# Kernel tuning notes

Measured on AMD Instinct MI355X. Metric: run time of the kernel, lower is better.

## Reference

```python
import jax, jax.numpy as jnp
import numpy as np


def _lstm(x, Wx, Wh, b):
    """Fused-gate LSTM over time axis 1. x: [B,T,I]; Wx: [I,4H]; Wh: [H,4H]; b: [4H].
    Gate order (i, f, g, o) as in flax.linen.LSTMCell. Zero initial carry."""
    B, T, _ = x.shape
    H = Wh.shape[0]
    # Precompute all input-to-gate contributions in one big GEMM.
    xg = jnp.einsum('bti,ih->bth', x, Wx) + b  # [B,T,4H]

    def step(carry, xt):
        c, h = carry
        z = xt + h @ Wh  # [B,4H]
        i, f, g, o = jnp.split(z, 4, axis=-1)
        c = jax.nn.sigmoid(f) * c + jax.nn.sigmoid(i) * jnp.tanh(g)
        h = jax.nn.sigmoid(o) * jnp.tanh(c)
        return (c, h), h

    init = (jnp.zeros((B, H), x.dtype), jnp.zeros((B, H), x.dtype))
    _, hs = jax.lax.scan(step, init, jnp.swapaxes(xg, 0, 1))  # hs: [T,B,H]
    return jnp.swapaxes(hs, 0, 1)  # [B,T,H]


def _forward(X, conv_w, conv_b,
             Wx1, Wh1, b1, Wx2, Wh2, b2, Wx3, Wh3, b3, Wx4, Wh4, b4,
             Wa, ba, Va, bva, Wd1, bd1, Wd2, bd2):
    # 1-D conv, SAME padding (flax default), NWC layout.
    x = jax.lax.conv_general_dilated(X, conv_w, (1,), 'SAME',
                                     dimension_numbers=('NWC', 'WIO', 'NWC')) + conv_b
    # NOTE: source uses jnp.flip(..., axis=-1) -> flips FEATURE axis (faithful to source).
    x1 = _lstm(x, Wx1, Wh1, b1)
    x2 = _lstm(jnp.flip(x, axis=-1), Wx2, Wh2, b2)
    x = jnp.concatenate([x1, x2], axis=-1)  # [B,T,2F]
    x1 = _lstm(x, Wx3, Wh3, b3)
    x2 = _lstm(jnp.flip(x, axis=-1), Wx4, Wh4, b4)
    enc = jnp.concatenate([x1, x2], axis=-1)  # [B,T,4F]
    # Additive attention: softmax over time axis.
    score = jnp.tanh(enc @ Wa + ba) @ Va + bva  # [B,T,1]
    w = jax.nn.softmax(score, axis=1)
    ctx = jnp.sum(w * enc, axis=1)  # [B,4F]
    # MLP head (dropout deterministic -> identity).
    h = jnp.tanh(ctx @ Wd1 + bd1)
    return h @ Wd2 + bd2  # [B,1]


def setup_inputs() -> dict:
    key = jax.random.key(0)
    B, T, Cin, F = 32, 4096, 8, 64
    ks = iter(jax.random.split(key, 32))

    def w(shape):
        fan_in = shape[0] if len(shape) <= 2 else shape[0] * shape[1]
        return jax.random.normal(next(ks), shape, jnp.float32) / np.sqrt(fan_in)

    d = {}
    d['X'] = jax.random.normal(next(ks), (B, T, Cin), jnp.float32)
    d['conv_w'] = w((4, Cin, 16))
    d['conv_b'] = jnp.zeros((16,), jnp.float32)
    lstm_dims = {'1': (16, F), '2': (16, F), '3': (2 * F, 2 * F), '4': (2 * F, 2 * F)}
    for n, (i_dim, h_dim) in lstm_dims.items():
        d['Wx' + n] = w((i_dim, 4 * h_dim))
        d['Wh' + n] = w((h_dim, 4 * h_dim))
        d['b' + n] = jnp.zeros((4 * h_dim,), jnp.float32)
    d['Wa'] = w((4 * F, F)); d['ba'] = jnp.zeros((F,), jnp.float32)
    d['Va'] = w((F, 1));     d['bva'] = jnp.zeros((1,), jnp.float32)
    d['Wd1'] = w((4 * F, F)); d['bd1'] = jnp.zeros((F,), jnp.float32)
    d['Wd2'] = w((F, 1));     d['bd2'] = jnp.zeros((1,), jnp.float32)
    d['deterministic'] = 1
    return d


def reference(X, conv_w, conv_b,
              Wx1, Wh1, b1, Wx2, Wh2, b2, Wx3, Wh3, b3, Wx4, Wh4, b4,
              Wa, ba, Va, bva, Wd1, bd1, Wd2, bd2, deterministic):
    # deterministic=1 -> dropout is the identity; already reflected in _forward.
    return _forward(X, conv_w, conv_b,
                    Wx1, Wh1, b1, Wx2, Wh2, b2, Wx3, Wh3, b3, Wx4, Wh4, b4,
                    Wa, ba, Va, bva, Wd1, bd1, Wd2, bd2)
```

## Files before the change

kernel.cpp:

```cpp
#include <hip/hip_runtime.h>


#define TFULL 4096
#define NB 32

__device__ __forceinline__ float fexp2(float x){ return __builtin_amdgcn_exp2f(x); }
__device__ __forceinline__ float frcp(float x){ return __builtin_amdgcn_rcpf(x); }
__device__ __forceinline__ float sigf(float x){ return frcp(1.f + fexp2(-1.44269504f*x)); }
__device__ __forceinline__ float tanh_(float x){
    float e = fexp2(fminf(2.88539008f*x, 126.f));
    return (e - 1.f) * frcp(e + 1.f);
}

__global__ __launch_bounds__(256) void k_init(float* __restrict__ st1,
        float* __restrict__ st2, float* __restrict__ am, float* __restrict__ al,
        float* __restrict__ acc){
    int i = blockIdx.x * 256 + threadIdx.x;
    if (i < 8192)  st1[i] = 0.f;
    if (i < 16384) st2[i] = 0.f;
    if (i < 8192)  acc[i] = 0.f;
    if (i < 32){ am[i] = -3.4e38f; al[i] = 0.f; }
}

__global__ __launch_bounds__(256) void k_pack(
        const float* __restrict__ Wx1, const float* __restrict__ Wh1, const float* __restrict__ b1,
        const float* __restrict__ Wx2, const float* __restrict__ Wh2, const float* __restrict__ b2,
        const float* __restrict__ Wx3, const float* __restrict__ Wh3, const float* __restrict__ b3,
        const float* __restrict__ Wx4, const float* __restrict__ Wh4, const float* __restrict__ b4,
        float* __restrict__ W34, float* __restrict__ b34, float* __restrict__ WhT2,
        float* __restrict__ WhT1, float* __restrict__ WxT1, float* __restrict__ b12){
    int i0 = blockIdx.x * 256 + threadIdx.x;
    int stride = gridDim.x * 256;
    for (int e = i0; e < 131072; e += stride){
        int k = e >> 10, n = e & 1023;
        W34[e] = (n < 512) ? Wx3[k*512 + n] : Wx4[(127 - k)*512 + (n - 512)];
    }
    for (int e = i0; e < 1024; e += stride) b34[e] = (e < 512) ? b3[e] : b4[e - 512];
    for (int e = i0; e < 131072; e += stride){
        int l = e >> 16, r = e & 65535, col = r >> 7, k = r & 127;
        WhT2[e] = (l ? Wh4 : Wh3)[k*512 + col];
    }
    for (int e = i0; e < 32768; e += stride){
        int l = e >> 14, r = e & 16383, col = r >> 6, k = r & 63;
        WhT1[e] = (l ? Wh2 : Wh1)[k*256 + col];
    }
    for (int e = i0; e < 8192; e += stride){
        int l = e >> 12, q = e & 4095, col = q >> 4, r = q & 15;
        WxT1[e] = l ? Wx2[(15 - r)*256 + col] : Wx1[r*256 + col];
    }
    for (int e = i0; e < 512; e += stride) b12[e] = (e < 256) ? b1[e] : b2[e - 256];
}

__global__ __launch_bounds__(256) void k_conv(const float* __restrict__ X,
        const float* __restrict__ W, const float* __restrict__ Bv,
        float* __restrict__ out, int t0, int lc){
    __shared__ float Ws[512];
    __shared__ float bs[16];
    int tid = threadIdx.x;
    Ws[tid] = W[tid]; Ws[tid + 256] = W[tid + 256];
    if (tid < 16) bs[tid] = Bv[tid];
    __syncthreads();
    int m = blockIdx.x * 256 + tid;
    int b = m >> lc, trel = m & ((1 << lc) - 1);
    int t = t0 + trel;
    float o[16];
    #pragma unroll
    for (int co = 0; co < 16; ++co) o[co] = bs[co];
    #pragma unroll
    for (int w = 0; w < 4; ++w){
        int tt = t + w - 1;
        if (tt >= 0 && tt < TFULL){
            const float* xr = X + ((size_t)(b << 12) + tt) * 8;
            #pragma unroll
            for (int ci = 0; ci < 8; ++ci){
                float v = xr[ci];
                #pragma unroll
                for (int co = 0; co < 16; ++co) o[co] += v * Ws[(w*8 + ci)*16 + co];
            }
        }
    }
    float* op = out + (size_t)m * 16;
    #pragma unroll
    for (int q = 0; q < 4; ++q)
        *(float4*)(op + q*4) = make_float4(o[q*4], o[q*4+1], o[q*4+2], o[q*4+3]);
}

__global__ void __launch_bounds__(512)
__attribute__((amdgpu_waves_per_eu(2, 2)))
k_scan1(const float* __restrict__ x,
        const float* __restrict__ WxT1, const float* __restrict__ WhT1,
        const float* __restrict__ b12,
        float* __restrict__ cc, float* __restrict__ st1, int C){
    int l = blockIdx.x >> 5;
    int b = blockIdx.x & 31;
    int j = threadIdx.x;
    int col = j & 255;
    int half = j >> 8;
    float4 wx4[4], wh4[8];
    float bias = 0.f;
    if (half == 0){
        const float4* wp = (const float4*)(WxT1 + ((size_t)l*256 + col)*16);
        #pragma unroll
        for (int i = 0; i < 4; ++i) wx4[i] = wp[i];
        bias = b12[l*256 + col];
    } else {
        #pragma unroll
        for (int i = 0; i < 4; ++i) wx4[i] = make_float4(0.f, 0.f, 0.f, 0.f);
    }
    {
        const float4* wp = (const float4*)(WhT1 + ((size_t)l*256 + col)*64 + half*32);
        #pragma unroll
        for (int i = 0; i < 8; ++i) wh4[i] = wp[i];
    }

    __shared__ float xs[128 * 16];
    __shared__ float zp[512];
    __shared__ float hbufs[64];
    float c = 0.f;
    int sidx = (l*32 + b)*64 + (j & 63);
    if (j < 64){ c = st1[sidx]; hbufs[j] = st1[4096 + sidx]; }
    __syncthreads();

    const float* xb = x + ((size_t)b * C) * 16;
    float* ccb = cc + ((size_t)b * C) * 128 + (l << 6);

    for (int t = 0; t < C; ++t){
        int s = t & 127;
        if (s == 0){
            __syncthreads();
            const float4* src = (const float4*)(xb + (size_t)t * 16);
            float4* dst = (float4*)xs;
            if (t + (j >> 2) < C) dst[j] = src[j];
            __syncthreads();
        }
        float a0 = bias, a1 = 0.f, a2 = 0.f, a3 = 0.f;
        if (half == 0){
            const float4* xr = (const float4*)(xs + s * 16);
            #pragma unroll
            for (int r4 = 0; r4 < 4; ++r4){
                float4 xv = xr[r4];
                a0 = fmaf(xv.x, wx4[r4].x, a0);
                a1 = fmaf(xv.y, wx4[r4].y, a1);
                a2 = fmaf(xv.z, wx4[r4].z, a2);
                a3 = fmaf(xv.w, wx4[r4].w, a3);
            }
        }
        const float4* hb4 = (const float4*)hbufs;
        #pragma unroll
        for (int k4 = 0; k4 < 8; ++k4){
            float4 hv = hb4[(half << 3) + k4];
            a0 = fmaf(hv.x, wh4[k4].x, a0);
            a1 = fmaf(hv.y, wh4[k4].y, a1);
            a2 = fmaf(hv.z, wh4[k4].z, a2);
            a3 = fmaf(hv.w, wh4[k4].w, a3);
        }
        zp[(half << 8) + col] = (a0 + a1) + (a2 + a3);
        __syncthreads();
        if (j < 64){
            float zi = zp[j]       + zp[256 + j];
            float zf = zp[64 + j]  + zp[320 + j];
            float zg = zp[128 + j] + zp[384 + j];
            float zo = zp[192 + j] + zp[448 + j];
            c = sigf(zf) * c + sigf(zi) * tanh_(zg);
            float h = sigf(zo) * tanh_(c);
            hbufs[j] = h;
            ccb[(size_t)t * 128 + j] = h;
        }
        __syncthreads();
    }
    if (j < 64){ st1[sidx] = c; st1[4096 + sidx] = hbufs[j]; }
}

template<bool TANH>
__global__ __launch_bounds__(128) void k_gemm(
        const float* __restrict__ A, int lda,
        const float* __restrict__ B, int ldb,
        const float* __restrict__ bias,
        float* __restrict__ Cm, int ldc, int K){
    __shared__ float As[64 * 129];
    __shared__ float Bs[64 * 68];
    int tid = threadIdx.x;
    int tx = tid & 7;
    int ty = tid >> 3;
    int r0 = blockIdx.x * 128;
    int n0 = blockIdx.y * 64;
    float acc[8][8];
    #pragma unroll
    for (int i = 0; i < 8; ++i)
        #pragma unroll
        for (int n = 0; n < 8; ++n) acc[i][n] = 0.f;

    for (int kb = 0; kb < K; kb += 64){
        __syncthreads();
        for (int idx = tid; idx < 2048; idx += 128){
            int r = idx >> 4, k4 = idx & 15;
            float4 v = *(const float4*)(A + (size_t)(r0 + r) * lda + kb + k4*4);
            As[(k4*4 + 0)*129 + r] = v.x;
            As[(k4*4 + 1)*129 + r] = v.y;
            As[(k4*4 + 2)*129 + r] = v.z;
            As[(k4*4 + 3)*129 + r] = v.w;
        }
        for (int idx = tid; idx < 1024; idx += 128){
            int n4 = idx & 15, k = idx >> 4;
            float4 v = *(const float4*)(B + (size_t)(kb + k) * ldb + n0 + n4*4);
            *(float4*)(Bs + k*68 + n4*4) = v;
        }
        __syncthreads();
        #pragma unroll 4
        for (int k = 0; k < 64; ++k){
            float a[8];
            #pragma unroll
            for (int i = 0; i < 8; ++i) a[i] = As[k*129 + ty*8 + i];
            float4 b0 = *(const float4*)(Bs + k*68 + tx*8);
            float4 b1 = *(const float4*)(Bs + k*68 + tx*8 + 4);
            float bq[8] = {b0.x, b0.y, b0.z, b0.w, b1.x, b1.y, b1.z, b1.w};
            #pragma unroll
            for (int i = 0; i < 8; ++i)
                #pragma unroll
                for (int n = 0; n < 8; ++n) acc[i][n] += a[i] * bq[n];
        }
    }
    #pragma unroll
    for (int i = 0; i < 8; ++i){
        size_t rr = (size_t)r0 + ty*8 + i;
        float* cp = Cm + rr * ldc + n0 + tx*8;
        float ov[8];
        #pragma unroll
        for (int n = 0; n < 8; ++n){
            float v = acc[i][n] + bias[n0 + tx*8 + n];
            ov[n] = TANH ? tanh_(v) : v;
        }
        *(float4*)cp       = make_float4(ov[0], ov[1], ov[2], ov[3]);
        *(float4*)(cp + 4) = make_float4(ov[4], ov[5], ov[6], ov[7]);
    }
}

__global__ void __launch_bounds__(1024)
__attribute__((amdgpu_waves_per_eu(4, 4)))
k_scan2(const float* __restrict__ xg, const float* __restrict__ WhT2,
        float* __restrict__ enc, float* __restrict__ st2, int C){
    int l = blockIdx.x >> 5;
    int b = blockIdx.x & 31;
    int j = threadIdx.x;
    int col = j & 511;
    int half = j >> 9;
    float4 wh4[16];
    {
        const float4* wp = (const float4*)(WhT2 + ((size_t)l*512 + col)*128 + half*64);
        #pragma unroll
        for (int i = 0; i < 16; ++i) wh4[i] = wp[i];
    }

    __shared__ float zp[1024];
    __shared__ float hbufs[128];
    float c = 0.f;
    int sidx = (l*32 + b)*128 + (j & 127);
    if (j < 128){ c = st2[sidx]; hbufs[j] = st2[8192 + sidx]; }
    __syncthreads();

    const float* xp = xg + ((size_t)b * C) * 1024 + (l << 9) + col;
    float* encb = enc + ((size_t)b * C) * 256 + (l << 7);

    float xnext = (half == 0) ? xp[0] : 0.f;
    for (int t = 0; t < C; ++t){
        float a0 = 0.f, a1 = 0.f, a2 = 0.f, a3 = 0.f;
        const float4* hb4 = (const float4*)hbufs;
        #pragma unroll
        for (int k4 = 0; k4 < 16; ++k4){
            float4 hv = hb4[(half << 4) + k4];
            a0 = fmaf(hv.x, wh4[k4].x, a0);
            a1 = fmaf(hv.y, wh4[k4].y, a1);
            a2 = fmaf(hv.z, wh4[k4].z, a2);
            a3 = fmaf(hv.w, wh4[k4].w, a3);
        }
        float z = (a0 + a1) + (a2 + a3);
        if (half == 0){
            z += xnext;
            int tn = (t + 1 < C) ? t + 1 : t;
            xnext = xp[(size_t)tn * 1024];
        }
        zp[(half << 9) + col] = z;
        __syncthreads();
        if (j < 128){
            float zi = zp[j]        + zp[512 + j];
            float zf = zp[128 + j]  + zp[640 + j];
            float zg = zp[256 + j]  + zp[768 + j];
            float zo = zp[384 + j]  + zp[896 + j];
            c = sigf(zf) * c + sigf(zi) * tanh_(zg);
            float h = sigf(zo) * tanh_(c);
            hbufs[j] = h;
            encb[(size_t)t * 256 + j] = h;
        }
        __syncthreads();
    }
    if (j < 128){ st2[sidx] = c; st2[8192 + sidx] = hbufs[j]; }
}

__global__ __launch_bounds__(256) void k_scorev(const float* __restrict__ u,
        const float* __restrict__ Va, const float* __restrict__ bva,
        float* __restrict__ sc){
    int m = blockIdx.x * 256 + threadIdx.x;
    const float4* up = (const float4*)(u + (size_t)m * 64);
    const float4* vp = (const float4*)Va;
    float acc = 0.f;
    #pragma unroll
    for (int i = 0; i < 16; ++i){
        float4 v = up[i], w = vp[i];
        acc += v.x*w.x + v.y*w.y + v.z*w.z + v.w*w.w;
    }
    sc[m] = acc + bva[0];
}

__global__ __launch_bounds__(1024) void k_attn(const float* __restrict__ sc,
        const float* __restrict__ enc, float* __restrict__ am,
        float* __restrict__ al, float* __restrict__ acc, int C){
    int b = blockIdx.x, tid = threadIdx.x;
    __shared__ float es[1024];
    __shared__ float red[16];
    __shared__ float sh[2];
    const float* sp = sc + (size_t)b * C;
    float mloc = -3.4e38f;
    for (int t = tid; t < C; t += 1024) mloc = fmaxf(mloc, sp[t]);
    #pragma unroll
    for (int off = 32; off; off >>= 1) mloc = fmaxf(mloc, __shfl_down(mloc, off));
    if ((tid & 63) == 0) red[tid >> 6] = mloc;
    __syncthreads();
    if (tid == 0){
        float mc = -3.4e38f;
        #pragma unroll
        for (int i = 0; i < 16; ++i) mc = fmaxf(mc, red[i]);
        float mo = am[b];
        float mn = fmaxf(mo, mc);
        sh[0] = mn;
        sh[1] = fexp2(1.44269504f * (mo - mn));
        am[b] = mn;
    }
    __syncthreads();
    float mn = sh[0], alpha = sh[1];
    float eloc = 0.f;
    for (int t = tid; t < C; t += 1024){
        float e = fexp2(1.44269504f * (sp[t] - mn));
        es[t] = e; eloc += e;
    }
    #pragma unroll
    for (int off = 32; off; off >>= 1) eloc += __shfl_down(eloc, off);
    if ((tid & 63) == 0) red[tid >> 6] = eloc;
    __syncthreads();
    if (tid == 0){
        float s = 0.f;
        #pragma unroll
        for (int i = 0; i < 16; ++i) s += red[i];
        al[b] = al[b] * alpha + s;
    }
    int jf = tid & 255, sl = tid >> 8;
    int tlen = C >> 2;
    const float* ep = enc + ((size_t)b * C + (size_t)sl * tlen) * 256 + jf;
    const float* eb = es + sl * tlen;
    float a = 0.f;
    for (int t = 0; t < tlen; ++t) a = fmaf(eb[t], ep[(size_t)t * 256], a);
    __syncthreads();
    es[tid] = a;
    __syncthreads();
    if (tid < 256)
        acc[b*256 + tid] = acc[b*256 + tid] * alpha
                         + ((es[tid] + es[256 + tid]) + (es[512 + tid] + es[768 + tid]));
}

__global__ __launch_bounds__(256) void k_head(const float* __restrict__ acc,
        const float* __restrict__ al,
        const float* __restrict__ Wd1, const float* __restrict__ bd1,
        const float* __restrict__ Wd2, const float* __restrict__ bd2,
        float* __restrict__ out){
    __shared__ float ctxs[32 * 256];
    __shared__ float h1s[32 * 64];
    int tid = threadIdx.x;
    for (int idx = tid; idx < 8192; idx += 256){
        int b = idx >> 8;
        ctxs[idx] = acc[idx] / al[b];
    }
    __syncthreads();
    for (int idx = tid; idx < 2048; idx += 256){
        int b = idx >> 6, n = idx & 63;
        float a = bd1[n];
        for (int i = 0; i < 256; ++i) a += ctxs[b*256 + i] * Wd1[i*64 + n];
        h1s[idx] = tanh_(a);
    }
    __syncthreads();
    if (tid < 32){
        float a = bd2[0];
        #pragma unroll
        for (int n = 0; n < 64; ++n) a += h1s[tid*64 + n] * Wd2[n];
        out[tid] = a;
    }
}

extern "C" void kernel_launch(void* const* d_in, const int* in_sizes, int n_in,
                              void* d_out, int out_size, void* d_ws, size_t ws_size,
                              hipStream_t stream){
    const float* X     = (const float*)d_in[0];
    const float* convw = (const float*)d_in[1];
    const float* convb = (const float*)d_in[2];
    const float* Wx1 = (const float*)d_in[3];
    const float* Wh1 = (const float*)d_in[4];
    const float* b1  = (const float*)d_in[5];
    const float* Wx2 = (const float*)d_in[6];
    const float* Wh2 = (const float*)d_in[7];
    const float* b2  = (const float*)d_in[8];
    const float* Wx3 = (const float*)d_in[9];
    const float* Wh3 = (const float*)d_in[10];
    const float* b3  = (const float*)d_in[11];
    const float* Wx4 = (const float*)d_in[12];
    const float* Wh4 = (const float*)d_in[13];
    const float* b4  = (const float*)d_in[14];
    const float* Wa  = (const float*)d_in[15];
    const float* ba  = (const float*)d_in[16];
    const float* Va  = (const float*)d_in[17];
    const float* bva = (const float*)d_in[18];
    const float* Wd1 = (const float*)d_in[19];
    const float* bd1 = (const float*)d_in[20];
    const float* Wd2 = (const float*)d_in[21];
    const float* bd2 = (const float*)d_in[22];
    float* out = (float*)d_out;
    (void)in_sizes; (void)n_in; (void)out_size;

    const size_t fixedFl = 131072 + 1024 + 131072 + 32768 + 8192 + 512
                         + 8192 + 16384 + 32 + 32 + 8192 + 32*1024;
    size_t capFl = ws_size / 4;
    int C = 1024;
    while (C > 32){
        size_t need = fixedFl + (size_t)NB * C * (16 + 128 + 1024 + 256 + 64);
        if (need <= capFl) break;
        C >>= 1;
    }
    int lc = 31 - __builtin_clz((unsigned)C);
    int nch = TFULL / C;

    float* ws   = (float*)d_ws;
    float* W34  = ws;
    float* b34  = W34 + 131072;
    float* WhT2 = b34 + 1024;
    float* WhT1 = WhT2 + 131072;
    float* WxT1 = WhT1 + 32768;
    float* b12  = WxT1 + 8192;
    float* st1  = b12 + 512;
    float* st2  = st1 + 8192;
    float* am   = st2 + 16384;
    float* al   = am + 32;
    float* acc  = al + 32;
    float* scb  = acc + 8192;
    float* xcv  = scb + 32*1024;
    float* ccb  = xcv + (size_t)NB*C*16;
    float* xgb  = ccb + (size_t)NB*C*128;
    float* enb  = xgb + (size_t)NB*C*1024;
    float* ub   = enb + (size_t)NB*C*256;

    k_init<<<64, 256, 0, stream>>>(st1, st2, am, al, acc);
    k_pack<<<512, 256, 0, stream>>>(Wx1, Wh1, b1, Wx2, Wh2, b2,
                                    Wx3, Wh3, b3, Wx4, Wh4, b4,
                                    W34, b34, WhT2, WhT1, WxT1, b12);

    for (int ch = 0; ch < nch; ++ch){
        int t0 = ch * C;
        k_conv<<<NB*C/256, 256, 0, stream>>>(X, convw, convb, xcv, t0, lc);
        k_scan1<<<64, 512, 0, stream>>>(xcv, WxT1, WhT1, b12, ccb, st1, C);
        k_gemm<false><<<dim3(NB*C/128, 16), 128, 0, stream>>>(
            ccb, 128, W34, 1024, b34, xgb, 1024, 128);
        k_scan2<<<64, 1024, 0, stream>>>(xgb, WhT2, enb, st2, C);
        k_gemm<true><<<dim3(NB*C/128, 1), 128, 0, stream>>>(
            enb, 256, Wa, 64, ba, ub, 64, 256);
        k_scorev<<<NB*C/256, 256, 0, stream>>>(ub, Va, bva, scb);
        k_attn<<<32, 1024, 0, stream>>>(scb, enb, am, al, acc, C);
    }
    k_head<<<1, 256, 0, stream>>>(acc, al, Wd1, bd1, Wd2, bd2, out);
}
```

Baseline: 6.388 ms.

## Split LSTM recurrence by K-slices with 4 gate columns per thread

Both recurrent scan kernels are restructured so each thread computes four adjacent gate columns over a K-slice, rather than one column over half of K. Weights are repacked into a per-thread contiguous layout and pinned in registers with empty asm. The 8 K-slice partial sums are reduced through shared memory by the cell-update threads. This aims to cut per-step LDS reads of h (float4 broadcasts reused across 4 columns) and improve register-resident weight use, at the cost of a larger 8-way shared-memory reduction on the serial critical path.

```diff
diff --git a/kernel.cpp b/kernel.cpp
--- a/kernel.cpp
+++ b/kernel.cpp
@@ -11,6 +11,7 @@
     float e = fexp2(fminf(2.88539008f*x, 126.f));
     return (e - 1.f) * frcp(e + 1.f);
 }
+#define PIN4(v) asm volatile("" : "+v"(v.x), "+v"(v.y), "+v"(v.z), "+v"(v.w))
 
 __global__ __launch_bounds__(256) void k_init(float* __restrict__ st1,
         float* __restrict__ st2, float* __restrict__ am, float* __restrict__ al,
@@ -27,8 +28,8 @@
         const float* __restrict__ Wx2, const float* __restrict__ Wh2, const float* __restrict__ b2,
         const float* __restrict__ Wx3, const float* __restrict__ Wh3, const float* __restrict__ b3,
         const float* __restrict__ Wx4, const float* __restrict__ Wh4, const float* __restrict__ b4,
-        float* __restrict__ W34, float* __restrict__ b34, float* __restrict__ WhT2,
-        float* __restrict__ WhT1, float* __restrict__ WxT1, float* __restrict__ b12){
+        float* __restrict__ W34, float* __restrict__ b34, float* __restrict__ W2p,
+        float* __restrict__ W1p, float* __restrict__ b12){
     int i0 = blockIdx.x * 256 + threadIdx.x;
     int stride = gridDim.x * 256;
     for (int e = i0; e < 131072; e += stride){
@@ -37,16 +38,24 @@
     }
     for (int e = i0; e < 1024; e += stride) b34[e] = (e < 512) ? b3[e] : b4[e - 512];
     for (int e = i0; e < 131072; e += stride){
-        int l = e >> 16, r = e & 65535, col = r >> 7, k = r & 127;
-        WhT2[e] = (l ? Wh4 : Wh3)[k*512 + col];
-    }
-    for (int e = i0; e < 32768; e += stride){
-        int l = e >> 14, r = e & 16383, col = r >> 6, k = r & 63;
-        WhT1[e] = (l ? Wh2 : Wh1)[k*256 + col];
-    }
-    for (int e = i0; e < 8192; e += stride){
-        int l = e >> 12, q = e & 4095, col = q >> 4, r = q & 15;
-        WxT1[e] = l ? Wx2[(15 - r)*256 + col] : Wx1[r*256 + col];
+        int l = e >> 16, r = e & 65535, tid = r >> 6, wq = r & 63;
+        int q = tid & 127, s = tid >> 7;
+        int c = wq >> 4, k = wq & 15;
+        W2p[e] = (l ? Wh4 : Wh3)[(s*16 + k)*512 + (4*q + c)];
+    }
+    for (int e = i0; e < 65536; e += stride){
+        int l = e >> 15, r = e & 32767, tid = r >> 6, wq = r & 63;
+        int q = tid & 63, s = tid >> 6;
+        float v = 0.f;
+        if (wq < 32){
+            int c = wq >> 3, k = wq & 7;
+            v = (l ? Wh2 : Wh1)[(s*8 + k)*256 + (4*q + c)];
+        } else if (s < 2){
+            int c = (wq - 32) >> 3, rr = (wq - 32) & 7;
+            int rg = s*8 + rr, col = 4*q + c;
+            v = l ? Wx2[(15 - rg)*256 + col] : Wx1[rg*256 + col];
+        }
+        W1p[e] = v;
     }
     for (int e = i0; e < 512; e += stride) b12[e] = (e < 256) ? b1[e] : b2[e - 256];
 }
@@ -85,90 +94,96 @@
         *(float4*)(op + q*4) = make_float4(o[q*4], o[q*4+1], o[q*4+2], o[q*4+3]);
 }
 
-__global__ void __launch_bounds__(512)
-__attribute__((amdgpu_waves_per_eu(2, 2)))
-k_scan1(const float* __restrict__ x,
-        const float* __restrict__ WxT1, const float* __restrict__ WhT1,
+__global__ void
+__attribute__((amdgpu_flat_work_group_size(512, 512), amdgpu_waves_per_eu(2, 2)))
+k_scan1(const float* __restrict__ x, const float* __restrict__ W1p,
         const float* __restrict__ b12,
         float* __restrict__ cc, float* __restrict__ st1, int C){
     int l = blockIdx.x >> 5;
     int b = blockIdx.x & 31;
-    int j = threadIdx.x;
-    int col = j & 255;
-    int half = j >> 8;
-    float4 wx4[4], wh4[8];
-    float bias = 0.f;
-    if (half == 0){
-        const float4* wp = (const float4*)(WxT1 + ((size_t)l*256 + col)*16);
-        #pragma unroll
-        for (int i = 0; i < 4; ++i) wx4[i] = wp[i];
-        bias = b12[l*256 + col];
-    } else {
-        #pragma unroll
-        for (int i = 0; i < 4; ++i) wx4[i] = make_float4(0.f, 0.f, 0.f, 0.f);
-    }
+    int tid = threadIdx.x;
+    int q = tid & 63;
+    int s = tid >> 6;
+    float4 w[16];
     {
-        const float4* wp = (const float4*)(WhT1 + ((size_t)l*256 + col)*64 + half*32);
-        #pragma unroll
-        for (int i = 0; i < 8; ++i) wh4[i] = wp[i];
+        const float4* wp = (const float4*)(W1p + ((size_t)l*512 + tid)*64);
+        #pragma unroll
+        for (int i = 0; i < 16; ++i) w[i] = wp[i];
+        #pragma unroll
+        for (int i = 0; i < 16; ++i) PIN4(w[i]);
+    }
+    float bi0 = 0.f, bi1 = 0.f, bi2 = 0.f, bi3 = 0.f;
+    if (tid < 64){
+        bi0 = b12[l*256 + tid];       bi1 = b12[l*256 + 64 + tid];
+        bi2 = b12[l*256 + 128 + tid]; bi3 = b12[l*256 + 192 + tid];
     }
 
     __shared__ float xs[128 * 16];
-    __shared__ float zp[512];
+    __shared__ float zp[8 * 256];
     __shared__ float hbufs[64];
     float c = 0.f;
-    int sidx = (l*32 + b)*64 + (j & 63);
-    if (j < 64){ c = st1[sidx]; hbufs[j] = st1[4096 + sidx]; }
+    int sidx = (l*32 + b)*64 + (tid & 63);
+    if (tid < 64){ c = st1[sidx]; hbufs[tid] = st1[4096 + sidx]; }
     __syncthreads();
 
     const float* xb = x + ((size_t)b * C) * 16;
     float* ccb = cc + ((size_t)b * C) * 128 + (l << 6);
 
     for (int t = 0; t < C; ++t){
-        int s = t & 127;
-        if (s == 0){
+        int st = t & 127;
+        if (st == 0){
             __syncthreads();
             const float4* src = (const float4*)(xb + (size_t)t * 16);
             float4* dst = (float4*)xs;
-            if (t + (j >> 2) < C) dst[j] = src[j];
+            if (t + (tid >> 2) < C) dst[tid] = src[tid];
             __syncthreads();
         }
-        float a0 = bias, a1 = 0.f, a2 = 0.f, a3 = 0.f;
-        if (half == 0){
-            const float4* xr = (const float4*)(xs + s * 16);
-            #pragma unroll
-            for (int r4 = 0; r4 < 4; ++r4){
+        float a0 = 0.f, a1 = 0.f, a2 = 0.f, a3 = 0.f;
+        const float4* hb4 = (const float4*)hbufs + (s << 1);
+        #pragma unroll
+        for (int k4 = 0; k4 < 2; ++k4){
+            float4 hv = hb4[k4];
+            a0 = fmaf(hv.x, w[k4].x, a0);     a0 = fmaf(hv.y, w[k4].y, a0);
+            a0 = fmaf(hv.z, w[k4].z, a0);     a0 = fmaf(hv.w, w[k4].w, a0);
+            a1 = fmaf(hv.x, w[2+k4].x, a1);   a1 = fmaf(hv.y, w[2+k4].y, a1);
+            a1 = fmaf(hv.z, w[2+k4].z, a1);   a1 = fmaf(hv.w, w[2+k4].w, a1);
+            a2 = fmaf(hv.x, w[4+k4].x, a2);   a2 = fmaf(hv.y, w[4+k4].y, a2);
+            a2 = fmaf(hv.z, w[4+k4].z, a2);   a2 = fmaf(hv.w, w[4+k4].w, a2);
+            a3 = fmaf(hv.x, w[6+k4].x, a3);   a3 = fmaf(hv.y, w[6+k4].y, a3);
+            a3 = fmaf(hv.z, w[6+k4].z, a3);   a3 = fmaf(hv.w, w[6+k4].w, a3);
+        }
+        if (s < 2){
+            const float4* xr = (const float4*)(xs + st * 16) + (s << 1);
+            #pragma unroll
+            for (int r4 = 0; r4 < 2; ++r4){
                 float4 xv = xr[r4];
-                a0 = fmaf(xv.x, wx4[r4].x, a0);
-                a1 = fmaf(xv.y, wx4[r4].y, a1);
-                a2 = fmaf(xv.z, wx4[r4].z, a2);
-                a3 = fmaf(xv.w, wx4[r4].w, a3);
+                a0 = fmaf(xv.x, w[8+r4].x, a0);    a0 = fmaf(xv.y, w[8+r4].y, a0);
+                a0 = fmaf(xv.z, w[8+r4].z, a0);    a0 = fmaf(xv.w, w[8+r4].w, a0);
+                a1 = fmaf(xv.x, w[10+r4].x, a1);   a1 = fmaf(xv.y, w[10+r4].y, a1);
+                a1 = fmaf(xv.z, w[10+r4].z, a1);   a1 = fmaf(xv.w, w[10+r4].w, a1);
+                a2 = fmaf(xv.x, w[12+r4].x, a2);   a2 = fmaf(xv.y, w[12+r4].y, a2);
+                a2 = fmaf(xv.z, w[12+r4].z, a2);   a2 = fmaf(xv.w, w[12+r4].w, a2);
+                a3 = fmaf(xv.x, w[14+r4].x, a3);   a3 = fmaf(xv.y, w[14+r4].y, a3);
+                a3 = fmaf(xv.z, w[14+r4].z, a3);   a3 = fmaf(xv.w, w[14+r4].w, a3);
             }
         }
-        const float4* hb4 = (const float4*)hbufs;
-        #pragma unroll
-        for (int k4 = 0; k4 < 8; ++k4){
-            float4 hv = hb4[(half << 3) + k4];
-            a0 = fmaf(hv.x, wh4[k4].x, a0);
-            a1 = fmaf(hv.y, wh4[k4].y, a1);
-            a2 = fmaf(hv.z, wh4[k4].z, a2);
-            a3 = fmaf(hv.w, wh4[k4].w, a3);
-        }
-        zp[(half << 8) + col] = (a0 + a1) + (a2 + a3);
-        __syncthreads();
-        if (j < 64){
-            float zi = zp[j]       + zp[256 + j];
-            float zf = zp[64 + j]  + zp[320 + j];
-            float zg = zp[128 + j] + zp[384 + j];
-            float zo = zp[192 + j] + zp[448 + j];
+        *(float4*)(zp + (s << 8) + (q << 2)) = make_float4(a0, a1, a2, a3);
+        __syncthreads();
+        if (tid < 64){
+            float zi = bi0, zf = bi1, zg = bi2, zo = bi3;
+            #pragma unroll
+            for (int ss = 0; ss < 8; ++ss){
+                const float* zr = zp + (ss << 8);
+                zi += zr[tid]; zf += zr[64 + tid]; zg += zr[128 + tid]; zo += zr[192 + tid];
+            }
             c = sigf(zf) * c + sigf(zi) * tanh_(zg);
             float h = sigf(zo) * tanh_(c);
-            hbufs[j] = h;
-            ccb[(size_t)t * 128 + j] = h;
-        }
-        __syncthreads();
-    }
-    if (j < 64){ st1[sidx] = c; st1[4096 + sidx] = hbufs[j]; }
+            hbufs[tid] = h;
+            ccb[(size_t)t * 128 + tid] = h;
+        }
+        __syncthreads();
+    }
+    if (tid < 64){ st1[sidx] = c; st1[4096 + sidx] = hbufs[tid]; }
 }
 
 template<bool TANH>
@@ -235,65 +250,73 @@
     }
 }
 
-__global__ void __launch_bounds__(1024)
-__attribute__((amdgpu_waves_per_eu(4, 4)))
-k_scan2(const float* __restrict__ xg, const float* __restrict__ WhT2,
+__global__ void
+__attribute__((amdgpu_flat_work_group_size(1024, 1024), amdgpu_waves_per_eu(4, 4)))
+k_scan2(const float* __restrict__ xg, const float* __restrict__ W2p,
         float* __restrict__ enc, float* __restrict__ st2, int C){
     int l = blockIdx.x >> 5;
     int b = blockIdx.x & 31;
-    int j = threadIdx.x;
-    int col = j & 511;
-    int half = j >> 9;
-    float4 wh4[16];
+    int tid = threadIdx.x;
+    int q = tid & 127;
+    int s = tid >> 7;
+    float4 w[16];
     {
-        const float4* wp = (const float4*)(WhT2 + ((size_t)l*512 + col)*128 + half*64);
-        #pragma unroll
-        for (int i = 0; i < 16; ++i) wh4[i] = wp[i];
-    }
-
-    __shared__ float zp[1024];
+        const float4* wp = (const float4*)(W2p + ((size_t)l*1024 + tid)*64);
+        #pragma unroll
+        for (int i = 0; i < 16; ++i) w[i] = wp[i];
+        #pragma unroll
+        for (int i = 0; i < 16; ++i) PIN4(w[i]);
+    }
+
+    __shared__ float zp[8 * 512];
     __shared__ float hbufs[128];
     float c = 0.f;
-    int sidx = (l*32 + b)*128 + (j & 127);
-    if (j < 128){ c = st2[sidx]; hbufs[j] = st2[8192 + sidx]; }
-    __syncthreads();
-
-    const float* xp = xg + ((size_t)b * C) * 1024 + (l << 9) + col;
+    int sidx = (l*32 + b)*128 + (tid & 127);
+    if (tid < 128){ c = st2[sidx]; hbufs[tid] = st2[8192 + sidx]; }
+    __syncthreads();
+
+    const float4* xp4 = (const float4*)(xg + ((size_t)b * C) * 1024 + (l << 9)) + q;
     float* encb = enc + ((size_t)b * C) * 256 + (l << 7);
 
-    float xnext = (half == 0) ? xp[0] : 0.f;
+    float4 xn = make_float4(0.f, 0.f, 0.f, 0.f);
+    if (s == 0) xn = xp4[0];
     for (int t = 0; t < C; ++t){
-        float a0 = 0.f, a1 = 0.f, a2 = 0.f, a3 = 0.f;
-        const float4* hb4 = (const float4*)hbufs;
-        #pragma unroll
-        for (int k4 = 0; k4 < 16; ++k4){
-            float4 hv = hb4[(half << 4) + k4];
-            a0 = fmaf(hv.x, wh4[k4].x, a0);
-            a1 = fmaf(hv.y, wh4[k4].y, a1);
-            a2 = fmaf(hv.z, wh4[k4].z, a2);
-            a3 = fmaf(hv.w, wh4[k4].w, a3);
-        }
-        float z = (a0 + a1) + (a2 + a3);
-        if (half == 0){
-            z += xnext;
+        float a0, a1, a2, a3;
+        if (s == 0){
+            a0 = xn.x; a1 = xn.y; a2 = xn.z; a3 = xn.w;
             int tn = (t + 1 < C) ? t + 1 : t;
-            xnext = xp[(size_t)tn * 1024];
-        }
-        zp[(half << 9) + col] = z;
-        __syncthreads();
-        if (j < 128){
-            float zi = zp[j]        + zp[512 + j];
-            float zf = zp[128 + j]  + zp[640 + j];
-            float zg = zp[256 + j]  + zp[768 + j];
-            float zo = zp[384 + j]  + zp[896 + j];
+            xn = xp4[(size_t)tn * 256];
+        } else { a0 = a1 = a2 = a3 = 0.f; }
+        const float4* hb4 = (const float4*)hbufs + (s << 2);
+        #pragma unroll
+        for (int k4 = 0; k4 < 4; ++k4){
+            float4 hv = hb4[k4];
+            a0 = fmaf(hv.x, w[k4].x, a0);      a0 = fmaf(hv.y, w[k4].y, a0);
+            a0 = fmaf(hv.z, w[k4].z, a0);      a0 = fmaf(hv.w, w[k4].w, a0);
+            a1 = fmaf(hv.x, w[4+k4].x, a1);    a1 = fmaf(hv.y, w[4+k4].y, a1);
+            a1 = fmaf(hv.z, w[4+k4].z, a1);    a1 = fmaf(hv.w, w[4+k4].w, a1);
+            a2 = fmaf(hv.x, w[8+k4].x, a2);    a2 = fmaf(hv.y, w[8+k4].y, a2);
+            a2 = fmaf(hv.z, w[8+k4].z, a2);    a2 = fmaf(hv.w, w[8+k4].w, a2);
+            a3 = fmaf(hv.x, w[12+k4].x, a3);   a3 = fmaf(hv.y, w[12+k4].y, a3);
+            a3 = fmaf(hv.z, w[12+k4].z, a3);   a3 = fmaf(hv.w, w[12+k4].w, a3);
+        }
+        *(float4*)(zp + (s << 9) + (q << 2)) = make_float4(a0, a1, a2, a3);
+        __syncthreads();
+        if (tid < 128){
+            float zi = 0.f, zf = 0.f, zg = 0.f, zo = 0.f;
+            #pragma unroll
+            for (int ss = 0; ss < 8; ++ss){
+                const float* zr = zp + (ss << 9);
+                zi += zr[tid]; zf += zr[128 + tid]; zg += zr[256 + tid]; zo += zr[384 + tid];
+            }
             c = sigf(zf) * c + sigf(zi) * tanh_(zg);
             float h = sigf(zo) * tanh_(c);
-            hbufs[j] = h;
-            encb[(size_t)t * 256 + j] = h;
-        }
-        __syncthreads();
-    }
-    if (j < 128){ st2[sidx] = c; st2[8192 + sidx] = hbufs[j]; }
+            hbufs[tid] = h;
+            encb[(size_t)t * 256 + tid] = h;
+        }
+        __syncthreads();
+    }
+    if (tid < 128){ st2[sidx] = c; st2[8192 + sidx] = hbufs[tid]; }
 }
 
 __global__ __launch_bounds__(256) void k_scorev(const float* __restrict__ u,
@@ -347,10 +370,10 @@
     if ((tid & 63) == 0) red[tid >> 6] = eloc;
     __syncthreads();
     if (tid == 0){
-        float s = 0.f;
-        #pragma unroll
-        for (int i = 0; i < 16; ++i) s += red[i];
-        al[b] = al[b] * alpha + s;
+        float sm = 0.f;
+        #pragma unroll
+        for (int i = 0; i < 16; ++i) sm += red[i];
+        al[b] = al[b] * alpha + sm;
     }
     int jf = tid & 255, sl = tid >> 8;
     int tlen = C >> 2;
@@ -423,7 +446,7 @@
     float* out = (float*)d_out;
     (void)in_sizes; (void)n_in; (void)out_size;
 
-    const size_t fixedFl = 131072 + 1024 + 131072 + 32768 + 8192 + 512
+    const size_t fixedFl = 131072 + 1024 + 131072 + 65536 + 512
                          + 8192 + 16384 + 32 + 32 + 8192 + 32*1024;
     size_t capFl = ws_size / 4;
     int C = 1024;
@@ -438,10 +461,9 @@
     float* ws   = (float*)d_ws;
     float* W34  = ws;
     float* b34  = W34 + 131072;
-    float* WhT2 = b34 + 1024;
-    float* WhT1 = WhT2 + 131072;
-    float* WxT1 = WhT1 + 32768;
-    float* b12  = WxT1 + 8192;
+    float* W2p  = b34 + 1024;
+    float* W1p  = W2p + 131072;
+    float* b12  = W1p + 65536;
     float* st1  = b12 + 512;
     float* st2  = st1 + 8192;
     float* am   = st2 + 16384;
@@ -457,15 +479,15 @@
     k_init<<<64, 256, 0, stream>>>(st1, st2, am, al, acc);
     k_pack<<<512, 256, 0, stream>>>(Wx1, Wh1, b1, Wx2, Wh2, b2,
                                     Wx3, Wh3, b3, Wx4, Wh4, b4,
-                                    W34, b34, WhT2, WhT1, WxT1, b12);
+                                    W34, b34, W2p, W1p, b12);
 
     for (int ch = 0; ch < nch; ++ch){
         int t0 = ch * C;
         k_conv<<<NB*C/256, 256, 0, stream>>>(X, convw, convb, xcv, t0, lc);
-        k_scan1<<<64, 512, 0, stream>>>(xcv, WxT1, WhT1, b12, ccb, st1, C);
+        k_scan1<<<64, 512, 0, stream>>>(xcv, W1p, b12, ccb, st1, C);
         k_gemm<false><<<dim3(NB*C/128, 16), 128, 0, stream>>>(
             ccb, 128, W34, 1024, b34, xgb, 1024, 128);
-        k_scan2<<<64, 1024, 0, stream>>>(xgb, WhT2, enb, st2, C);
+        k_scan2<<<64, 1024, 0, stream>>>(xgb, W2p, enb, st2, C);
         k_gemm<true><<<dim3(NB*C/128, 1), 128, 0, stream>>>(
             enb, 256, Wa, 64, ba, ub, 64, 256);
         k_scorev<<<NB*C/256, 256, 0, stream>>>(ub, Va, bva, scb);
```

New measurement: 5.979 ms. 1.07x faster.
